# Kernel tuning notes

Measured on AMD Instinct MI355X. Metric: run time of the kernel, lower is better.

Reference implementation:

```python
import jax, jax.numpy as jnp
import numpy as np
from math import sqrt

KEY_DIM = 128
VALUE_DIM = 128
SUMMARY_DIM = 128
QUESTION_NUM = 10000
CONCEPT_NUM = 64
B = 128
S = 128


def setup_inputs() -> dict:
    key = jax.random.key(0)
    ks = jax.random.split(key, 24)
    stdev = 1.0 / sqrt(CONCEPT_NUM + KEY_DIM)

    def lin_w(k, out_f, in_f):
        bound = 1.0 / sqrt(in_f)
        return jax.random.uniform(k, (out_f, in_f), jnp.float32, -bound, bound)

    def lin_b(k, out_f, in_f):
        bound = 1.0 / sqrt(in_f)
        return jax.random.uniform(k, (out_f,), jnp.float32, -bound, bound)

    q_emb = jax.random.normal(ks[0], (QUESTION_NUM + 1, KEY_DIM), jnp.float32)
    q_emb = q_emb.at[0].set(0.0)  # padding_idx = 0
    i_emb = jax.random.normal(ks[1], (2 * QUESTION_NUM + 1, VALUE_DIM), jnp.float32)
    i_emb = i_emb.at[0].set(0.0)

    inp = {
        "right_input": jax.random.randint(ks[2], (B, S), 0, 2 * QUESTION_NUM + 1),
        "wrong_input": jax.random.randint(ks[3], (B, S), 0, 2 * QUESTION_NUM + 1),
        "target_id": jax.random.randint(ks[4], (B,), 0, QUESTION_NUM + 1),
        "q_emb": q_emb,
        "i_emb": i_emb,
        "key_W": lin_w(ks[5], CONCEPT_NUM, KEY_DIM),  # no bias
        "erase_W": lin_w(ks[6], VALUE_DIM, VALUE_DIM),
        "erase_b": lin_b(ks[7], VALUE_DIM, VALUE_DIM),
        "add_W": lin_w(ks[8], VALUE_DIM, VALUE_DIM),
        "add_b": lin_b(ks[9], VALUE_DIM, VALUE_DIM),
        "rsum_W": lin_w(ks[10], SUMMARY_DIM, VALUE_DIM + KEY_DIM),
        "rsum_b": lin_b(ks[11], SUMMARY_DIM, VALUE_DIM + KEY_DIM),
        "wsum_W": lin_w(ks[12], SUMMARY_DIM, VALUE_DIM + KEY_DIM),
        "wsum_b": lin_b(ks[13], SUMMARY_DIM, VALUE_DIM + KEY_DIM),
        "succ_W": lin_w(ks[14], 1, SUMMARY_DIM),
        "succ_b": lin_b(ks[15], 1, SUMMARY_DIM),
        "fail_W": lin_w(ks[16], 1, SUMMARY_DIM),
        "fail_b": lin_b(ks[17], 1, SUMMARY_DIM),
        "diff_W": lin_w(ks[18], 1, KEY_DIM),
        "diff_b": lin_b(ks[19], 1, KEY_DIM),
        "right_mem_init": jax.random.uniform(ks[20], (VALUE_DIM, CONCEPT_NUM), jnp.float32, -stdev, stdev),
        "wrong_mem_init": jax.random.uniform(ks[21], (VALUE_DIM, CONCEPT_NUM), jnp.float32, -stdev, stdev),
    }
    return inp


def reference(right_input, wrong_input, target_id, q_emb, i_emb, key_W,
              erase_W, erase_b, add_W, add_b, rsum_W, rsum_b, wsum_W, wsum_b,
              succ_W, succ_b, fail_W, fail_b, diff_W, diff_b,
              right_mem_init, wrong_mem_init):
    Q = (i_emb.shape[0] - 1) // 2
    batch = right_input.shape[0]

    def corr(qid):  # (B,) -> (B, C) correlation weights
        return jax.nn.softmax(q_emb[qid] @ key_W.T, axis=-1)

    def update(mem, inter):
        # mem: (B, V, C); inter: (B,) interaction ids
        vec = i_emb[inter]                                  # (B, V)
        e = jax.nn.sigmoid(vec @ erase_W.T + erase_b)       # (B, V)
        a = jnp.tanh(vec @ add_W.T + add_b)                 # (B, V)
        qid = inter - Q * (inter > Q).astype(inter.dtype)
        w = corr(qid)                                       # (B, C)
        # erase/add are outer products w (x) e, w (x) a -> (B, V, C)
        return mem * (1.0 - e[:, :, None] * w[:, None, :]) + a[:, :, None] * w[:, None, :]

    def step(carry, xs):
        rm, wm = carry
        ri, wi = xs
        return (update(rm, ri), update(wm, wi)), None

    rm0 = jnp.broadcast_to(right_mem_init, (batch,) + right_mem_init.shape)
    wm0 = jnp.broadcast_to(wrong_mem_init, (batch,) + wrong_mem_init.shape)
    (rm, wm), _ = jax.lax.scan(step, (rm0, wm0), (right_input.T, wrong_input.T))

    qv = q_emb[target_id]                                   # (B, K)
    w_t = corr(target_id)                                   # (B, C)
    right_read = jnp.einsum('bvc,bc->bv', rm, w_t)          # (B, V)
    wrong_read = jnp.einsum('bvc,bc->bv', wm, w_t)

    r_sum = jnp.tanh(jnp.concatenate([right_read, qv], axis=-1) @ rsum_W.T + rsum_b)
    w_sum = jnp.tanh(jnp.concatenate([wrong_read, qv], axis=-1) @ wsum_W.T + wsum_b)

    success_level = jnp.tanh(r_sum @ succ_W.T + succ_b)     # (B, 1)
    failure_level = jnp.tanh(w_sum @ fail_W.T + fail_b)     # (B, 1)
    difficulty_level = jnp.tanh(qv @ diff_W.T + diff_b)     # (B, 1)

    success_count = jnp.sum(jnp.clip(right_input, 0, 1)).astype(jnp.float32)
    failure_count = jnp.sum(jnp.clip(wrong_input, 0, 1)).astype(jnp.float32)

    out = (success_level * jax.nn.sigmoid(success_count)
           + failure_level * jax.nn.sigmoid(failure_count)
           - difficulty_level * 2.0)
    return out
```

## Files before the change

kernel.cpp:

```cpp
#include <hip/hip_runtime.h>
#include <hip/hip_bf16.h>

#define BB 128
#define SS 128
#define VD 128
#define CN 64
#define KD 128
#define QN 10000
#define MROWS (2*BB*SS)
#define MTOT  (MROWS + BB)

typedef __attribute__((ext_vector_type(8))) short bf16x8;
typedef __attribute__((ext_vector_type(4))) float f32x4;
typedef __attribute__((ext_vector_type(2))) float f32x2;

__device__ __forceinline__ float bflo(unsigned int u) { return __uint_as_float(u << 16); }
__device__ __forceinline__ float bfhi(unsigned int u) { return __uint_as_float(u & 0xffff0000u); }
__device__ __forceinline__ unsigned short f2bf(float f) {
    unsigned int x = __float_as_uint(f);
    return (unsigned short)((x + 0x7fffu + ((x >> 16) & 1u)) >> 16);
}
__device__ __forceinline__ unsigned int pk2(float lo, float hi) {
    return (unsigned int)f2bf(lo) | ((unsigned int)f2bf(hi) << 16);
}
__device__ __forceinline__ float fast_tanh(float x) {
    float e = __expf(2.0f * x);
    return 1.0f - 2.0f / (e + 1.0f);
}
__device__ __forceinline__ float fast_sig(float x) {
    return 1.0f / (1.0f + __expf(-x));
}

__global__ __launch_bounds__(256) void k_wcnt(
    const float* __restrict__ erase_W, const float* __restrict__ add_W,
    const float* __restrict__ key_W, unsigned short* __restrict__ Bfrag,
    const int* __restrict__ ri, const int* __restrict__ wi, float* __restrict__ sig)
{
    if (blockIdx.x < 20) {
        const int bid = blockIdx.x * 4 + (threadIdx.x >> 6);
        const int l = threadIdx.x & 63;
        const int n = (bid >> 2) * 16 + (l & 15);
        const int k0 = (bid & 3) * 32 + (l >> 4) * 8;
        const float* src;
        if (n < 128)      src = erase_W + (size_t)n * KD + k0;
        else if (n < 256) src = add_W + (size_t)(n - 128) * KD + k0;
        else              src = key_W + (size_t)(n - 256) * KD + k0;
        float4 fa = ((const float4*)src)[0];
        float4 fb = ((const float4*)src)[1];
        uint4 o = make_uint4(pk2(fa.x, fa.y), pk2(fa.z, fa.w), pk2(fb.x, fb.y), pk2(fb.z, fb.w));
        *(uint4*)(Bfrag + ((size_t)bid * 64 + l) * 8) = o;
    } else {
        __shared__ int sr_s[4], sw_s[4];
        const int t = threadIdx.x;
        const int4* r4 = (const int4*)ri;
        const int4* w4 = (const int4*)wi;
        int sr = 0, sw = 0;
        #pragma unroll 4
        for (int p = 0; p < 16; ++p) {
            int4 a = r4[p * 256 + t];
            int4 b = w4[p * 256 + t];
            sr += (a.x >= 1) + (a.y >= 1) + (a.z >= 1) + (a.w >= 1);
            sw += (b.x >= 1) + (b.y >= 1) + (b.z >= 1) + (b.w >= 1);
        }
        for (int off = 1; off < 64; off <<= 1) { sr += __shfl_xor(sr, off); sw += __shfl_xor(sw, off); }
        int wid = t >> 6;
        if ((t & 63) == 0) { sr_s[wid] = sr; sw_s[wid] = sw; }
        __syncthreads();
        if (t == 0) {
            int SR = sr_s[0]+sr_s[1]+sr_s[2]+sr_s[3];
            int SW = sw_s[0]+sw_s[1]+sw_s[2]+sw_s[3];
            sig[0] = 1.0f / (1.0f + __expf(-(float)SR));
            sig[1] = 1.0f / (1.0f + __expf(-(float)SW));
        }
    }
}

__global__ __launch_bounds__(256) void k_mfma(
    const int* __restrict__ ri, const int* __restrict__ wi, const int* __restrict__ tgt,
    const float* __restrict__ q_emb, const float* __restrict__ i_emb,
    const float* __restrict__ erase_b, const float* __restrict__ add_b,
    const unsigned short* __restrict__ Bfrag,
    unsigned short* __restrict__ EAbuf,
    float* __restrict__ Wf, float* __restrict__ WTbuf)
{
    __shared__ __align__(16) char shA[32 * 256];
    __shared__ __align__(16) char shB[32 * 68 * 4];
    __shared__ int id_s[32], ir_s[32];

    const int t = threadIdx.x;
    const int lane = t & 63;
    const int w = t >> 6;
    const int base = blockIdx.x * 32;
    const bool ea = (base < MROWS);

    if (t < 32) {
        int r = base + t;
        int irow = 0, qid;
        if (r < MROWS) {
            int m = r >> 14;
            int idx = r & 16383;
            int inter = (m == 0) ? ri[idx] : wi[idx];
            irow = inter;
            qid = (inter > QN) ? inter - QN : inter;
        } else {
            qid = tgt[r - MROWS];
        }
        id_s[t] = qid; ir_s[t] = irow;
    }
    __syncthreads();

    {
        const int r = t >> 3, o = t & 7;
        const int bb = r * 256 + o * 32;
        const int sw = (r & 7) << 4;
        {
            const float* src = q_emb + (size_t)id_s[r] * KD + o * 16;
            float4 f0 = ((const float4*)src)[0];
            float4 f1 = ((const float4*)src)[1];
            float4 f2 = ((const float4*)src)[2];
            float4 f3 = ((const float4*)src)[3];
            *(uint4*)(shB + (bb ^ sw))        = make_uint4(pk2(f0.x,f0.y), pk2(f0.z,f0.w), pk2(f1.x,f1.y), pk2(f1.z,f1.w));
            *(uint4*)(shB + ((bb + 16) ^ sw)) = make_uint4(pk2(f2.x,f2.y), pk2(f2.z,f2.w), pk2(f3.x,f3.y), pk2(f3.z,f3.w));
        }
        if (ea) {
            const float* src = i_emb + (size_t)ir_s[r] * KD + o * 16;
            float4 f0 = ((const float4*)src)[0];
            float4 f1 = ((const float4*)src)[1];
            float4 f2 = ((const float4*)src)[2];
            float4 f3 = ((const float4*)src)[3];
            *(uint4*)(shA + (bb ^ sw))        = make_uint4(pk2(f0.x,f0.y), pk2(f0.z,f0.w), pk2(f1.x,f1.y), pk2(f1.z,f1.w));
            *(uint4*)(shA + ((bb + 16) ^ sw)) = make_uint4(pk2(f2.x,f2.y), pk2(f2.z,f2.w), pk2(f3.x,f3.y), pk2(f3.z,f3.w));
        }
    }
    __syncthreads();

    const int rowl = lane & 15;
    const int kb16 = (lane >> 4) * 16;

    bf16x8 afQ[2][4];
    #pragma unroll
    for (int mt = 0; mt < 2; ++mt)
        #pragma unroll
        for (int kt = 0; kt < 4; ++kt) {
            int row = mt * 16 + rowl;
            int addr = (row * 256 + kt * 64 + kb16) ^ ((row & 7) << 4);
            afQ[mt][kt] = *(const bf16x8*)(shB + addr);
        }

    f32x4 accK0 = {0.f,0.f,0.f,0.f}, accK1 = {0.f,0.f,0.f,0.f};
    {
        const int gk = 16 + w;
        #pragma unroll
        for (int kt = 0; kt < 4; ++kt) {
            bf16x8 bf = *(const bf16x8*)(Bfrag + ((size_t)(gk * 4 + kt) * 64 + lane) * 8);
            accK0 = __builtin_amdgcn_mfma_f32_16x16x32_bf16(afQ[0][kt], bf, accK0, 0, 0, 0);
            accK1 = __builtin_amdgcn_mfma_f32_16x16x32_bf16(afQ[1][kt], bf, accK1, 0, 0, 0);
        }
    }
    __syncthreads();

    {
        float* L = (float*)shB;
        const int col = w * 16 + rowl;
        const int rb4 = (lane >> 4) * 4;
        #pragma unroll
        for (int rr = 0; rr < 4; ++rr) L[(rb4 + rr) * 68 + col] = accK0[rr];
        #pragma unroll
        for (int rr = 0; rr < 4; ++rr) L[(16 + rb4 + rr) * 68 + col] = accK1[rr];
    }
    __syncthreads();

    {
        const float* L = (const float*)shB;
        const int rr = t >> 3, q = t & 7;
        float4 va = *(const float4*)(L + rr * 68 + q * 8);
        float4 vb = *(const float4*)(L + rr * 68 + q * 8 + 4);
        float mx = fmaxf(fmaxf(fmaxf(va.x, va.y), fmaxf(va.z, va.w)),
                         fmaxf(fmaxf(vb.x, vb.y), fmaxf(vb.z, vb.w)));
        #pragma unroll
        for (int off = 1; off < 8; off <<= 1) mx = fmaxf(mx, __shfl_xor(mx, off));
        float e0 = __expf(va.x - mx), e1 = __expf(va.y - mx), e2 = __expf(va.z - mx), e3 = __expf(va.w - mx);
        float e4 = __expf(vb.x - mx), e5 = __expf(vb.y - mx), e6 = __expf(vb.z - mx), e7 = __expf(vb.w - mx);
        float s = e0 + e1 + e2 + e3 + e4 + e5 + e6 + e7;
        #pragma unroll
        for (int off = 1; off < 8; off <<= 1) s += __shfl_xor(s, off);
        float inv = 1.0f / s;
        int R = base + rr;
        if (R < MROWS) {
            float* dw = Wf + (size_t)R * CN + q * 8;
            *(float4*)dw       = make_float4(e0*inv, e1*inv, e2*inv, e3*inv);
            *(float4*)(dw + 4) = make_float4(e4*inv, e5*inv, e6*inv, e7*inv);
        } else {
            float* dst = WTbuf + (size_t)(R - MROWS) * CN + q * 8;
            *(float4*)dst       = make_float4(e0*inv, e1*inv, e2*inv, e3*inv);
            *(float4*)(dst + 4) = make_float4(e4*inv, e5*inv, e6*inv, e7*inv);
        }
    }

    if (ea) {
        bf16x8 afI[2][4];
        #pragma unroll
        for (int mt = 0; mt < 2; ++mt)
            #pragma unroll
            for (int kt = 0; kt < 4; ++kt) {
                int row = mt * 16 + rowl;
                int addr = (row * 256 + kt * 64 + kb16) ^ ((row & 7) << 4);
                afI[mt][kt] = *(const bf16x8*)(shA + addr);
            }

        const int rb4 = (lane >> 4) * 4;
        #pragma unroll
        for (int gi = 0; gi < 4; ++gi) {
            const int g = w + gi * 4;
            f32x4 a0 = {0.f,0.f,0.f,0.f}, a1 = {0.f,0.f,0.f,0.f};
            #pragma unroll
            for (int kt = 0; kt < 4; ++kt) {
                bf16x8 bf = *(const bf16x8*)(Bfrag + ((size_t)(g * 4 + kt) * 64 + lane) * 8);
                a0 = __builtin_amdgcn_mfma_f32_16x16x32_bf16(afI[0][kt], bf, a0, 0, 0, 0);
                a1 = __builtin_amdgcn_mfma_f32_16x16x32_bf16(afI[1][kt], bf, a1, 0, 0, 0);
            }
            const bool isE = (g < 8);
            const int cc = (g & 7) * 16 + rowl;
            const float bv = isE ? erase_b[cc] : add_b[cc];
            const int off = isE ? 0 : 1;
            #pragma unroll
            for (int mt = 0; mt < 2; ++mt) {
                f32x4 av = mt ? a1 : a0;
                #pragma unroll
                for (int rr = 0; rr < 4; ++rr) {
                    float x = av[rr] + bv;
                    float y = isE ? fast_sig(x) : fast_tanh(x);
                    EAbuf[((size_t)(base + mt * 16 + rb4 + rr) * VD + cc) * 2 + off] = f2bf(y);
                }
            }
        }
    }
}

__global__ __launch_bounds__(512, 4) void k_scan(
    const unsigned int* __restrict__ EAbuf, const float* __restrict__ Wf,
    const float* __restrict__ WTbuf,
    const float* __restrict__ rmem0, const float* __restrict__ wmem0,
    float* __restrict__ readbuf)
{
    __shared__ unsigned int lds_ea[SS * VD];
    __shared__ float lds_w[SS * 32];
    const int t = threadIdx.x;
    const int chain = blockIdx.x & 255;
    const int chalf = blockIdx.x >> 8;
    const int m  = chain >> 7;
    const int b  = chain & 127;
    const int ck2 = t >> 7;
    const int v  = t & 127;
    const int c0l = ck2 * 8;

    {
        const uint4* sEA = (const uint4*)(EAbuf + (size_t)chain * SS * VD);
        uint4* dEA = (uint4*)lds_ea;
        #pragma unroll
        for (int i = 0; i < 8; ++i) dEA[t + i * 512] = sEA[t + i * 512];
        const float* sW = Wf + (size_t)chain * SS * CN + chalf * 32;
        float4* dW = (float4*)lds_w;
        #pragma unroll
        for (int i = 0; i < 2; ++i) {
            int idx = t + i * 512;
            int s = idx >> 3, q = idx & 7;
            dW[idx] = *(const float4*)(sW + (size_t)s * CN + q * 4);
        }
    }

    const float* minit = (m == 0) ? rmem0 : wmem0;
    f32x2 mm[4];
    #pragma unroll
    for (int j = 0; j < 4; ++j) {
        mm[j].x = minit[v * CN + chalf * 32 + c0l + 2*j];
        mm[j].y = minit[v * CN + chalf * 32 + c0l + 2*j + 1];
    }
    __syncthreads();

    #pragma unroll 8
    for (int s = 0; s < SS; ++s) {
        unsigned int u = lds_ea[s * VD + v];
        float e = bflo(u), a = bfhi(u);
        const float* wp = lds_w + s * 32 + c0l;
        float4 w0 = *(const float4*)wp;
        float4 w1 = *(const float4*)(wp + 4);
        f32x2 ev = {e, e}, av = {a, a}, g, wv;
        g = av - ev * mm[0]; wv.x = w0.x; wv.y = w0.y; mm[0] += wv * g;
        g = av - ev * mm[1]; wv.x = w0.z; wv.y = w0.w; mm[1] += wv * g;
        g = av - ev * mm[2]; wv.x = w1.x; wv.y = w1.y; mm[2] += wv * g;
        g = av - ev * mm[3]; wv.x = w1.z; wv.y = w1.w; mm[3] += wv * g;
    }

    const float* wt = WTbuf + (size_t)b * CN + chalf * 32 + c0l;
    float4 wa = *(const float4*)wt;
    float4 wb = *(const float4*)(wt + 4);
    float p = 0.0f;
    p = fmaf(mm[0].x, wa.x, p); p = fmaf(mm[0].y, wa.y, p);
    p = fmaf(mm[1].x, wa.z, p); p = fmaf(mm[1].y, wa.w, p);
    p = fmaf(mm[2].x, wb.x, p); p = fmaf(mm[2].y, wb.y, p);
    p = fmaf(mm[3].x, wb.z, p); p = fmaf(mm[3].y, wb.w, p);
    __syncthreads();
    lds_w[ck2 * 128 + v] = p;
    __syncthreads();
    if (t < 128) {
        float s = lds_w[t] + lds_w[128 + t] + lds_w[256 + t] + lds_w[384 + t];
        readbuf[((size_t)chalf * 256 + chain) * VD + t] = s;
    }
}

__global__ __launch_bounds__(256) void k_head(
    const float* __restrict__ readbuf, const int* __restrict__ tgt,
    const float* __restrict__ q_emb,
    const float* __restrict__ rsum_W, const float* __restrict__ rsum_b,
    const float* __restrict__ wsum_W, const float* __restrict__ wsum_b,
    const float* __restrict__ succ_W, const float* __restrict__ succ_b,
    const float* __restrict__ fail_W, const float* __restrict__ fail_b,
    const float* __restrict__ diff_W, const float* __restrict__ diff_b,
    const float* __restrict__ sig, float* __restrict__ out)
{
    __shared__ float xr[256], xw[256];
    __shared__ float part[2][128];
    __shared__ float red_s[6];
    const int t = threadIdx.x;
    const int j = t & 127;
    const int h = t >> 7;
    const int b = blockIdx.x;
    if (h == 0) {
        int tid_ = tgt[b];
        float qv = q_emb[(size_t)tid_ * KD + j];
        xr[j]       = readbuf[(size_t)b * VD + j] + readbuf[(size_t)(256 + b) * VD + j];
        xr[128 + j] = qv;
        xw[j]       = readbuf[(size_t)(BB + b) * VD + j] + readbuf[(size_t)(256 + BB + b) * VD + j];
        xw[128 + j] = qv;
    }
    __syncthreads();

    float rs = (h == 0) ? rsum_b[j] : 0.0f;
    float wv = (h == 0) ? wsum_b[j] : 0.0f;
    const float* rw = rsum_W + (size_t)j * 256 + h * 128;
    const float* ww = wsum_W + (size_t)j * 256 + h * 128;
    const float* xrp = xr + h * 128;
    const float* xwp = xw + h * 128;
    #pragma unroll 4
    for (int k = 0; k < 128; ++k) {
        rs = fmaf(rw[k], xrp[k], rs);
        wv = fmaf(ww[k], xwp[k], wv);
    }
    if (h == 1) { part[0][j] = rs; part[1][j] = wv; }
    __syncthreads();
    if (h == 0) {
        rs += part[0][j];
        wv += part[1][j];
        float r_sum = fast_tanh(rs), w_sum = fast_tanh(wv);
        float qv = xr[128 + j];
        float ps = r_sum * succ_W[j];
        float pf = w_sum * fail_W[j];
        float pd = qv    * diff_W[j];
        for (int off = 1; off < 64; off <<= 1) {
            ps += __shfl_xor(ps, off);
            pf += __shfl_xor(pf, off);
            pd += __shfl_xor(pd, off);
        }
        int wid = j >> 6;
        if ((j & 63) == 0) { red_s[wid*3+0] = ps; red_s[wid*3+1] = pf; red_s[wid*3+2] = pd; }
    }
    __syncthreads();
    if (t == 0) {
        float Ps = red_s[0] + red_s[3];
        float Pf = red_s[1] + red_s[4];
        float Pd = red_s[2] + red_s[5];
        float succ = fast_tanh(Ps + succ_b[0]);
        float fail = fast_tanh(Pf + fail_b[0]);
        float diff = fast_tanh(Pd + diff_b[0]);
        out[b] = succ * sig[0] + fail * sig[1] - 2.0f * diff;
    }
}

extern "C" void kernel_launch(void* const* d_in, const int* in_sizes, int n_in,
                              void* d_out, int out_size, void* d_ws, size_t ws_size,
                              hipStream_t stream) {
    const int*   ri      = (const int*)d_in[0];
    const int*   wi      = (const int*)d_in[1];
    const int*   tgt     = (const int*)d_in[2];
    const float* q_emb   = (const float*)d_in[3];
    const float* i_emb   = (const float*)d_in[4];
    const float* key_W   = (const float*)d_in[5];
    const float* erase_W = (const float*)d_in[6];
    const float* erase_b = (const float*)d_in[7];
    const float* add_W   = (const float*)d_in[8];
    const float* add_b   = (const float*)d_in[9];
    const float* rsum_W  = (const float*)d_in[10];
    const float* rsum_b  = (const float*)d_in[11];
    const float* wsum_W  = (const float*)d_in[12];
    const float* wsum_b  = (const float*)d_in[13];
    const float* succ_W  = (const float*)d_in[14];
    const float* succ_b  = (const float*)d_in[15];
    const float* fail_W  = (const float*)d_in[16];
    const float* fail_b  = (const float*)d_in[17];
    const float* diff_W  = (const float*)d_in[18];
    const float* diff_b  = (const float*)d_in[19];
    const float* rmem0   = (const float*)d_in[20];
    const float* wmem0   = (const float*)d_in[21];

    char* ws = (char*)d_ws;
    unsigned short* EAbuf   = (unsigned short*)(ws + 0);
    float*          Wf      = (float*)(ws + 16777216);
    float*          WTbuf   = (float*)(ws + 25165824);
    float*          readbuf = (float*)(ws + 25198592);
    unsigned short* Bfrag   = (unsigned short*)(ws + 25460736);
    float*          sig     = (float*)(ws + 25542656);
    float*          out     = (float*)d_out;

    hipLaunchKernelGGL(k_wcnt, dim3(21), dim3(256), 0, stream,
        erase_W, add_W, key_W, Bfrag, ri, wi, sig);
    hipLaunchKernelGGL(k_mfma, dim3(1028), dim3(256), 0, stream,
        ri, wi, tgt, q_emb, i_emb, erase_b, add_b, Bfrag,
        EAbuf, Wf, WTbuf);
    hipLaunchKernelGGL(k_scan, dim3(512), dim3(512), 0, stream,
        (const unsigned int*)EAbuf, Wf, WTbuf, rmem0, wmem0, readbuf);
    hipLaunchKernelGGL(k_head, dim3(128), dim3(256), 0, stream,
        readbuf, tgt, q_emb, rsum_W, rsum_b, wsum_W, wsum_b,
        succ_W, succ_b, fail_W, fail_b, diff_W, diff_b, sig, out);
}
```

Measured before the change: 61.39 us.

## Pack erase/add into single 32-bit stores and broadcast scan weights via readlane

In k_mfma, each wave now computes both the erase and add MFMA tiles for the same columns before its epilogue. It then writes one packed 32-bit erase/add pair per element instead of two separate 16-bit scattered stores. In k_scan, the per-step correlation weights are no longer staged in LDS. Each lane preloads two timesteps of weights into registers, and readlane broadcasts them inside the scan loop, removing the LDS weight reads and the scalar pair-vector math. This trades LDS traffic for many scalar readlane ops and more registers, and the loop loses its 2-wide packed FMAs.

Measured after the change: 68.00 us. 10.8% more time.

```diff
diff --git a/kernel.cpp b/kernel.cpp
--- a/kernel.cpp
+++ b/kernel.cpp
@@ -12,7 +12,6 @@
 
 typedef __attribute__((ext_vector_type(8))) short bf16x8;
 typedef __attribute__((ext_vector_type(4))) float f32x4;
-typedef __attribute__((ext_vector_type(2))) float f32x2;
 
 __device__ __forceinline__ float bflo(unsigned int u) { return __uint_as_float(u << 16); }
 __device__ __forceinline__ float bfhi(unsigned int u) { return __uint_as_float(u & 0xffff0000u); }
@@ -80,7 +79,7 @@
     const float* __restrict__ q_emb, const float* __restrict__ i_emb,
     const float* __restrict__ erase_b, const float* __restrict__ add_b,
     const unsigned short* __restrict__ Bfrag,
-    unsigned short* __restrict__ EAbuf,
+    unsigned int* __restrict__ EAbuf,
     float* __restrict__ Wf, float* __restrict__ WTbuf)
 {
     __shared__ __align__(16) char shA[32 * 256];
@@ -209,6 +208,7 @@
             }
 
         const int rb4 = (lane >> 4) * 4;
+        f32x4 accE[2][2], accA[2][2];
         #pragma unroll
         for (int gi = 0; gi < 4; ++gi) {
             const int g = w + gi * 4;
@@ -219,18 +219,21 @@
                 a0 = __builtin_amdgcn_mfma_f32_16x16x32_bf16(afI[0][kt], bf, a0, 0, 0, 0);
                 a1 = __builtin_amdgcn_mfma_f32_16x16x32_bf16(afI[1][kt], bf, a1, 0, 0, 0);
             }
-            const bool isE = (g < 8);
-            const int cc = (g & 7) * 16 + rowl;
-            const float bv = isE ? erase_b[cc] : add_b[cc];
-            const int off = isE ? 0 : 1;
+            if (gi < 2) { accE[gi][0] = a0; accE[gi][1] = a1; }
+            else        { accA[gi - 2][0] = a0; accA[gi - 2][1] = a1; }
+        }
+        #pragma unroll
+        for (int ci = 0; ci < 2; ++ci) {
+            const int cc = ci * 64 + w * 16 + rowl;
+            const float bvE = erase_b[cc];
+            const float bvA = add_b[cc];
             #pragma unroll
             for (int mt = 0; mt < 2; ++mt) {
-                f32x4 av = mt ? a1 : a0;
                 #pragma unroll
                 for (int rr = 0; rr < 4; ++rr) {
-                    float x = av[rr] + bv;
-                    float y = isE ? fast_sig(x) : fast_tanh(x);
-                    EAbuf[((size_t)(base + mt * 16 + rb4 + rr) * VD + cc) * 2 + off] = f2bf(y);
+                    float e = fast_sig(accE[ci][mt][rr] + bvE);
+                    float a = fast_tanh(accA[ci][mt][rr] + bvA);
+                    EAbuf[(size_t)(base + mt * 16 + rb4 + rr) * VD + cc] = pk2(e, a);
                 }
             }
         }
@@ -244,7 +247,7 @@
     float* __restrict__ readbuf)
 {
     __shared__ unsigned int lds_ea[SS * VD];
-    __shared__ float lds_w[SS * 32];
+    __shared__ float psum[4 * 128];
     const int t = threadIdx.x;
     const int chain = blockIdx.x & 255;
     const int chalf = blockIdx.x >> 8;
@@ -252,59 +255,60 @@
     const int b  = chain & 127;
     const int ck2 = t >> 7;
     const int v  = t & 127;
-    const int c0l = ck2 * 8;
+    const int lane = t & 63;
+    const int c0 = chalf * 32 + ck2 * 8;
 
     {
         const uint4* sEA = (const uint4*)(EAbuf + (size_t)chain * SS * VD);
         uint4* dEA = (uint4*)lds_ea;
         #pragma unroll
         for (int i = 0; i < 8; ++i) dEA[t + i * 512] = sEA[t + i * 512];
-        const float* sW = Wf + (size_t)chain * SS * CN + chalf * 32;
-        float4* dW = (float4*)lds_w;
-        #pragma unroll
-        for (int i = 0; i < 2; ++i) {
-            int idx = t + i * 512;
-            int s = idx >> 3, q = idx & 7;
-            dW[idx] = *(const float4*)(sW + (size_t)s * CN + q * 4);
-        }
-    }
+    }
+
+    const float* wsrc = Wf + ((size_t)chain * SS + 2 * lane) * CN + c0;
+    float4 wr0 = *(const float4*)(wsrc);
+    float4 wr1 = *(const float4*)(wsrc + 4);
+    float4 wr2 = *(const float4*)(wsrc + CN);
+    float4 wr3 = *(const float4*)(wsrc + CN + 4);
+    float w_reg[16] = { wr0.x, wr0.y, wr0.z, wr0.w, wr1.x, wr1.y, wr1.z, wr1.w,
+                        wr2.x, wr2.y, wr2.z, wr2.w, wr3.x, wr3.y, wr3.z, wr3.w };
 
     const float* minit = (m == 0) ? rmem0 : wmem0;
-    f32x2 mm[4];
-    #pragma unroll
-    for (int j = 0; j < 4; ++j) {
-        mm[j].x = minit[v * CN + chalf * 32 + c0l + 2*j];
-        mm[j].y = minit[v * CN + chalf * 32 + c0l + 2*j + 1];
-    }
-    __syncthreads();
-
-    #pragma unroll 8
-    for (int s = 0; s < SS; ++s) {
-        unsigned int u = lds_ea[s * VD + v];
-        float e = bflo(u), a = bfhi(u);
-        const float* wp = lds_w + s * 32 + c0l;
-        float4 w0 = *(const float4*)wp;
-        float4 w1 = *(const float4*)(wp + 4);
-        f32x2 ev = {e, e}, av = {a, a}, g, wv;
-        g = av - ev * mm[0]; wv.x = w0.x; wv.y = w0.y; mm[0] += wv * g;
-        g = av - ev * mm[1]; wv.x = w0.z; wv.y = w0.w; mm[1] += wv * g;
-        g = av - ev * mm[2]; wv.x = w1.x; wv.y = w1.y; mm[2] += wv * g;
-        g = av - ev * mm[3]; wv.x = w1.z; wv.y = w1.w; mm[3] += wv * g;
-    }
-
-    const float* wt = WTbuf + (size_t)b * CN + chalf * 32 + c0l;
+    float4 m0 = *(const float4*)(minit + v * CN + c0);
+    float4 m1 = *(const float4*)(minit + v * CN + c0 + 4);
+    float mm[8] = { m0.x, m0.y, m0.z, m0.w, m1.x, m1.y, m1.z, m1.w };
+
+    __syncthreads();
+
+    for (int so = 0; so < 16; ++so) {
+        #pragma unroll
+        for (int k = 0; k < 8; ++k) {
+            const int s = so * 8 + k;
+            unsigned int u = lds_ea[s * VD + v];
+            float e = bflo(u), a = bfhi(u);
+            const int sl = s >> 1;
+            #pragma unroll
+            for (int j = 0; j < 8; ++j) {
+                float wv = __uint_as_float(__builtin_amdgcn_readlane(
+                    (int)__float_as_uint(w_reg[(k & 1) * 8 + j]), sl));
+                float g = fmaf(-e, mm[j], a);
+                mm[j] = fmaf(wv, g, mm[j]);
+            }
+        }
+    }
+
+    const float* wt = WTbuf + (size_t)b * CN + c0;
     float4 wa = *(const float4*)wt;
     float4 wb = *(const float4*)(wt + 4);
     float p = 0.0f;
-    p = fmaf(mm[0].x, wa.x, p); p = fmaf(mm[0].y, wa.y, p);
-    p = fmaf(mm[1].x, wa.z, p); p = fmaf(mm[1].y, wa.w, p);
-    p = fmaf(mm[2].x, wb.x, p); p = fmaf(mm[2].y, wb.y, p);
-    p = fmaf(mm[3].x, wb.z, p); p = fmaf(mm[3].y, wb.w, p);
-    __syncthreads();
-    lds_w[ck2 * 128 + v] = p;
+    p = fmaf(mm[0], wa.x, p); p = fmaf(mm[1], wa.y, p);
+    p = fmaf(mm[2], wa.z, p); p = fmaf(mm[3], wa.w, p);
+    p = fmaf(mm[4], wb.x, p); p = fmaf(mm[5], wb.y, p);
+    p = fmaf(mm[6], wb.z, p); p = fmaf(mm[7], wb.w, p);
+    psum[ck2 * 128 + v] = p;
     __syncthreads();
     if (t < 128) {
-        float s = lds_w[t] + lds_w[128 + t] + lds_w[256 + t] + lds_w[384 + t];
+        float s = psum[t] + psum[128 + t] + psum[256 + t] + psum[384 + t];
         readbuf[((size_t)chalf * 256 + chain) * VD + t] = s;
     }
 }
@@ -404,7 +408,7 @@
     const float* wmem0   = (const float*)d_in[21];
 
     char* ws = (char*)d_ws;
-    unsigned short* EAbuf   = (unsigned short*)(ws + 0);
+    unsigned int*   EAbuf   = (unsigned int*)(ws + 0);
     float*          Wf      = (float*)(ws + 16777216);
     float*          WTbuf   = (float*)(ws + 25165824);
     float*          readbuf = (float*)(ws + 25198592);
@@ -418,7 +422,7 @@
         ri, wi, tgt, q_emb, i_emb, erase_b, add_b, Bfrag,
         EAbuf, Wf, WTbuf);
     hipLaunchKernelGGL(k_scan, dim3(512), dim3(512), 0, stream,
-        (const unsigned int*)EAbuf, Wf, WTbuf, rmem0, wmem0, readbuf);
+        EAbuf, Wf, WTbuf, rmem0, wmem0, readbuf);
     hipLaunchKernelGGL(k_head, dim3(128), dim3(256), 0, stream,
         readbuf, tgt, q_emb, rsum_W, rsum_b, wsum_W, wsum_b,
         succ_W, succ_b, fail_W, fail_b, diff_W, diff_b, sig, out);
```
